# Kernel tuning notes

Measured on AMD Instinct MI355X. Metric: run time of the kernel, lower is better.

Reference implementation:

```python
import jax, jax.numpy as jnp
import numpy as np

D_MODEL = 512
D_K = 64
D_V = 128
H = D_MODEL // D_V  # 4 heads (num_head = d_model // d_v per the source)
B, N = 4, 2048


def setup_inputs() -> dict:
    key = jax.random.key(0)
    k0, k1, k2, k3, k4 = jax.random.split(key, 5)
    s = 0.02
    return {
        "input_x": jax.random.normal(k0, (B, N, D_MODEL), jnp.float32),
        "Wq": jax.random.normal(k1, (D_MODEL, H * D_K), jnp.float32) * s,
        "Wk": jax.random.normal(k2, (D_MODEL, H * D_K), jnp.float32) * s,
        "Wv": jax.random.normal(k3, (D_MODEL, D_MODEL), jnp.float32) * s,
        "Wo": jax.random.normal(k4, (D_MODEL, D_MODEL), jnp.float32) * s,
    }


def reference(input_x, Wq, Wk, Wv, Wo):
    b, n, _ = input_x.shape
    # Contiguous per-head slices in the source == a simple reshape here.
    q = (input_x @ Wq).reshape(b, n, H, D_K)   # [B,N,H,dk]
    k = (input_x @ Wk).reshape(b, n, H, D_K)   # [B,N,H,dk]
    v = (input_x @ Wv).reshape(b, n, H, D_V)   # [B,N,H,dv]
    scale = jnp.sqrt(jnp.float32(D_K))
    scores = jnp.einsum('bqhd,bkhd->bhqk', q, k) / scale  # [B,H,N,N]
    # FAITHFUL quirk: the source uses nn.Softmax() with no dim on a 3D
    # (B,N,N) tensor; PyTorch's legacy dim inference picks dim=0 (batch).
    attn = jax.nn.softmax(scores, axis=0)
    out = jnp.einsum('bhqk,bkhd->bqhd', attn, v).reshape(b, n, H * D_V)
    return out @ Wo
```

## Files before the change

### kernel.cpp

```cpp
#include <hip/hip_runtime.h>
#include <hip/hip_bf16.h>


typedef __attribute__((ext_vector_type(8))) short short8;
typedef __attribute__((ext_vector_type(4))) float floatx4;
typedef unsigned short u16;
typedef unsigned int u32;

#define MFMA16(a, b, c) __builtin_amdgcn_mfma_f32_16x16x32_bf16((a), (b), (c), 0, 0, 0)

__device__ __forceinline__ u16 f2bf(float f) {
    union { float f; unsigned u; } v; v.f = f;
    unsigned r = v.u + 0x7fffu + ((v.u >> 16) & 1u);
    return (u16)(r >> 16);
}

__device__ __forceinline__ float bf2f(u16 b) {
    union { unsigned u; float f; } v; v.u = ((u32)b) << 16;
    return v.f;
}

__device__ __forceinline__ u32 pk2bf(float a, float b) {
#if __has_builtin(__builtin_amdgcn_cvt_pk_bf16_f32)
    typedef __attribute__((ext_vector_type(2))) __bf16 bf16x2;
    union { bf16x2 v; u32 u; } c;
    c.v = __builtin_amdgcn_cvt_pk_bf16_f32(a, b);
    return c.u;
#else
    return (u32)f2bf(a) | ((u32)f2bf(b) << 16);
#endif
}

__device__ __forceinline__ float ex2(float x) {
#if __has_builtin(__builtin_amdgcn_exp2f)
    return __builtin_amdgcn_exp2f(x);
#else
    return exp2f(x);
#endif
}

__device__ __forceinline__ void gload_lds16(const u16* g, u16* l) {
    __builtin_amdgcn_global_load_lds(
        (const __attribute__((address_space(1))) void*)(const void*)g,
        (__attribute__((address_space(3))) void*)(void*)l, 16, 0, 0);
}

__global__ __launch_bounds__(256) void prep_all_kernel(
    const float* __restrict__ x, u16* __restrict__ xb,
    const float* __restrict__ Wq, const float* __restrict__ Wk,
    const float* __restrict__ Wv, const float* __restrict__ Wo,
    u16* __restrict__ WallT, u16* __restrict__ WoT) {
    const int bid = blockIdx.x;
    const int tid = threadIdx.x;
    if (bid < 4096) {
        int i = bid * 256 + tid;
        float4 v = ((const float4*)x)[i];
        ushort4 o;
        o.x = f2bf(v.x); o.y = f2bf(v.y); o.z = f2bf(v.z); o.w = f2bf(v.w);
        ((ushort4*)xb)[i] = o;
        return;
    }
    __shared__ u16 lds[64 * 80];
    const int t = bid - 4096;
    const int k0 = (t & 7) * 64;
    const int n0 = (t >> 3) * 64;
    const float* src; int ld, coff; float scale = 1.0f;
    u16* dst;
    if (n0 < 256)       { src = Wq; ld = 256; coff = n0;        dst = WallT + (size_t)n0 * 512; scale = 0.18033688011f; }
    else if (n0 < 512)  { src = Wk; ld = 256; coff = n0 - 256;  dst = WallT + (size_t)n0 * 512; }
    else if (n0 < 1024) { src = Wv; ld = 512; coff = n0 - 512;  dst = WallT + (size_t)n0 * 512; }
    else                { src = Wo; ld = 512; coff = n0 - 1024; dst = WoT + (size_t)(n0 - 1024) * 512; }
#pragma unroll
    for (int p = 0; p < 4; p++) {
        int r  = (tid >> 4) + p * 16;
        int c4 = (tid & 15) * 4;
        float4 v = *(const float4*)&src[(size_t)(k0 + r) * ld + coff + c4];
        lds[(c4 + 0) * 80 + r] = f2bf(v.x * scale);
        lds[(c4 + 1) * 80 + r] = f2bf(v.y * scale);
        lds[(c4 + 2) * 80 + r] = f2bf(v.z * scale);
        lds[(c4 + 3) * 80 + r] = f2bf(v.w * scale);
    }
    __syncthreads();
#pragma unroll
    for (int p = 0; p < 2; p++) {
        int nn = (tid >> 3) + p * 32;
        int kk = (tid & 7) * 8;
        *(short8*)&dst[(size_t)nn * 512 + k0 + kk] = *(const short8*)&lds[nn * 80 + kk];
    }
}

__global__ __launch_bounds__(512) void gemm_qkv_kernel(
    const u16* __restrict__ A, const u16* __restrict__ BT,
    u16* __restrict__ Qp, u16* __restrict__ Kp, u16* __restrict__ Vp,
    int Kdim) {
    __shared__ u16 sm[16896];
    u16* Asl = sm;
    u16* Bsl = sm + 8192;
    const int tid = threadIdx.x;
    const int bid0 = blockIdx.y * 8 + blockIdx.x;
    const int xcd = bid0 & 7, jj = bid0 >> 3;
    const int mbase = (xcd * 8 + (jj >> 3)) * 128;
    const int nbase = (jj & 7) * 128;
    const int wave = tid >> 6, lane = tid & 63;
    const int wm = wave >> 2, wn = wave & 3;
    const int lq = lane & 15, quad = lane >> 4;

    const int scol = ((lane & 7) ^ (lane >> 3)) * 8;
    const u16* gA = A + (size_t)(mbase + wave * 16 + (lane >> 3)) * Kdim + scol;
    const u16* gB = BT + (size_t)(nbase + wave * 16 + (lane >> 3)) * Kdim + scol;
    u16* lA = &Asl[(wave * 16) * 64];
    u16* lB = &Bsl[(wave * 16) * 64];

    const floatx4 z4 = {0.f, 0.f, 0.f, 0.f};
    floatx4 acc[4][2];
#pragma unroll
    for (int i = 0; i < 4; i++)
#pragma unroll
        for (int j = 0; j < 2; j++) acc[i][j] = z4;

    const int nk = Kdim >> 6;
    for (int kk = 0; kk < nk; kk++) {
        const int kb = kk << 6;
        if (kk) __syncthreads();
#pragma unroll
        for (int i = 0; i < 2; i++) {
            gload_lds16(gA + kb + (size_t)(i * 8) * Kdim, lA + (i * 8) * 64);
            gload_lds16(gB + kb + (size_t)(i * 8) * Kdim, lB + (i * 8) * 64);
        }
        __syncthreads();
#pragma unroll
        for (int ki = 0; ki < 2; ki++) {
            short8 af[4], bf[2];
#pragma unroll
            for (int mi = 0; mi < 4; mi++)
                af[mi] = *(const short8*)&Asl[(wm * 64 + mi * 16 + lq) * 64 +
                                              (((ki * 4 + quad) ^ (lq & 7)) * 8)];
#pragma unroll
            for (int ni = 0; ni < 2; ni++)
                bf[ni] = *(const short8*)&Bsl[(wn * 32 + ni * 16 + lq) * 64 +
                                              (((ki * 4 + quad) ^ (lq & 7)) * 8)];
#pragma unroll
            for (int mi = 0; mi < 4; mi++)
#pragma unroll
                for (int ni = 0; ni < 2; ni++)
                    acc[mi][ni] = MFMA16(af[mi], bf[ni], acc[mi][ni]);
        }
    }
    __syncthreads();
    const bool vtile = (nbase >= 512);
#pragma unroll
    for (int mi = 0; mi < 4; mi++)
#pragma unroll
        for (int ni = 0; ni < 2; ni++) {
            int cl = wn * 32 + ni * 16 + lq;
#pragma unroll
            for (int r = 0; r < 4; r++) {
                int rl = wm * 64 + mi * 16 + quad * 4 + r;
                if (vtile) sm[cl * 132 + rl] = f2bf(acc[mi][ni][r]);
                else       sm[rl * 132 + cl] = f2bf(acc[mi][ni][r]);
            }
        }
    __syncthreads();
    const int b = mbase >> 11;
    const int keyb = mbase & 2047;
    if (nbase < 256) {
        const int hq = nbase >> 6;
        const int qs_base = keyb >> 4;
#pragma unroll
        for (int t = 0; t < 4; t++) {
            int l = wave * 4 + t;
            int qs2 = l >> 2, h2 = (l >> 1) & 1, ki = l & 1;
            int qd = lane >> 4, lqq = lane & 15;
            short8 v = *(const short8*)&sm[(qs2 * 16 + lqq) * 132 + h2 * 64 + ki * 32 + qd * 8];
            int h = hq + h2;
            size_t base = ((size_t)(((b * 4 + h) * 128 + (qs_base + qs2)) * 2 + ki) * 64 + lane) << 3;
            *(short8*)&Qp[base] = v;
        }
    } else if (nbase < 512) {
        const int hb = (nbase - 256) >> 6;
        const int ktb = keyb >> 6;
#pragma unroll
        for (int t = 0; t < 4; t++) {
            int l = wave * 4 + t;
            int kt2 = l >> 4, hf = (l >> 3) & 1, nj = (l >> 2) & 1;
            int h2 = (l >> 1) & 1, ki = l & 1;
            int quadk = lane >> 4, lqk = lane & 15;
            short8 v = *(const short8*)&sm[(kt2 * 64 + hf * 32 + lqk * 2 + nj) * 132 +
                                           h2 * 64 + ki * 32 + quadk * 8];
            int h = hb + h2;
            size_t base = ((size_t)(((((b * 4 + h) * 32 + (ktb + kt2)) * 2 + hf) * 2 + nj)
                                    * 2 + ki) * 64 + lane) << 3;
            *(short8*)&Kp[base] = v;
        }
    } else {
        const int h = (nbase - 512) >> 7;
        const int ktb = keyb >> 6;
#pragma unroll
        for (int t = 0; t < 4; t++) {
            int l = wave * 4 + t;
            int kt2 = l >> 4, hf = (l >> 3) & 1, niv = (l >> 1) & 3, wv = l & 1;
            int quadv = lane >> 4, lqv = lane & 15;
            short8 v = *(const short8*)&sm[(hf * 64 + niv * 16 + lqv) * 132 +
                                           kt2 * 64 + wv * 32 + quadv * 8];
            size_t base = ((size_t)(((((b * 4 + h) * 32 + (ktb + kt2)) * 2 + hf) * 4 + niv)
                                    * 2 + wv) * 64 + lane) << 3;
            *(short8*)&Vp[base] = v;
        }
    }
}

__global__ __launch_bounds__(512) void gemm_out_kernel(
    const u16* __restrict__ A, const u16* __restrict__ BT,
    float* __restrict__ Cf, int Kdim, int ldc) {
    __shared__ u16 Asl[64 * 64];
    __shared__ u16 Bsl[128 * 64];
    const int tid = threadIdx.x;
    const int bid0 = blockIdx.y * 4 + blockIdx.x;
    const int xcd = bid0 & 7, jj = bid0 >> 3;
    const int mbase = (xcd * 16 + (jj >> 2)) * 64;
    const int nbase = (jj & 3) * 128;
    const int wave = tid >> 6, lane = tid & 63;
    const int wm = wave >> 2, wn = wave & 3;
    const int lq = lane & 15, quad = lane >> 4;
    const size_t S = (size_t)8192 * 512;

    const u16* gA = A + (size_t)(mbase + wave * 8 + (lane >> 3)) * Kdim + (lane & 7) * 8;
    const u16* gB = BT + (size_t)(nbase + wave * 16 + (lane >> 3)) * Kdim +
                    (((lane & 7) ^ (lane >> 3)) * 8);
    u16* lAw = &Asl[(wave * 8 + (lane >> 3)) * 64 + (((lane & 7) ^ (lane >> 3)) * 8)];
    u16* lB = &Bsl[(wave * 16) * 64];

    const floatx4 z4 = {0.f, 0.f, 0.f, 0.f};
    floatx4 acc[2][2];
#pragma unroll
    for (int i = 0; i < 2; i++)
#pragma unroll
        for (int j = 0; j < 2; j++) acc[i][j] = z4;

    const int nk = Kdim >> 6;
    for (int kk = 0; kk < nk; kk++) {
        const int kb = kk << 6;
        short8 p0 = *(const short8*)(gA + kb);
        short8 p1 = *(const short8*)(gA + kb + S);
        short8 p2 = *(const short8*)(gA + kb + 2 * S);
        short8 p3 = *(const short8*)(gA + kb + 3 * S);
        if (kk) __syncthreads();
        gload_lds16(gB + kb, lB);
        gload_lds16(gB + kb + (size_t)8 * Kdim, lB + 8 * 64);
        short8 o;
#pragma unroll
        for (int j2 = 0; j2 < 8; j2++) {
            float s = bf2f((u16)p0[j2]) + bf2f((u16)p1[j2]) +
                      bf2f((u16)p2[j2]) + bf2f((u16)p3[j2]);
            o[j2] = (short)f2bf(s);
        }
        *(short8*)lAw = o;
        __syncthreads();
#pragma unroll
        for (int ki = 0; ki < 2; ki++) {
            short8 af[2], bf[2];
#pragma unroll
            for (int mi = 0; mi < 2; mi++)
                af[mi] = *(const short8*)&Asl[(wm * 32 + mi * 16 + lq) * 64 +
                                              (((ki * 4 + quad) ^ (lq & 7)) * 8)];
#pragma unroll
            for (int ni = 0; ni < 2; ni++)
                bf[ni] = *(const short8*)&Bsl[(wn * 32 + ni * 16 + lq) * 64 +
                                              (((ki * 4 + quad) ^ (lq & 7)) * 8)];
#pragma unroll
            for (int mi = 0; mi < 2; mi++)
#pragma unroll
                for (int ni = 0; ni < 2; ni++)
                    acc[mi][ni] = MFMA16(af[mi], bf[ni], acc[mi][ni]);
        }
    }
#pragma unroll
    for (int mi = 0; mi < 2; mi++)
#pragma unroll
        for (int ni = 0; ni < 2; ni++)
#pragma unroll
            for (int r = 0; r < 4; r++)
                Cf[(size_t)(mbase + wm * 32 + mi * 16 + quad * 4 + r) * ldc +
                   (nbase + wn * 32 + ni * 16 + lq)] = acc[mi][ni][r];
}

__global__ __launch_bounds__(512) void attn_kernel(const u16* __restrict__ Qp,
                                                   const u16* __restrict__ Kp,
                                                   const u16* __restrict__ Vp,
                                                   u16* __restrict__ Pp) {
    __shared__ u16 pl[2 * 4 * 4096];
    const int bx = blockIdx.x;
    const int h = bx & 3;
    const int ck = (bx >> 2) & 3;
    const int qt = bx >> 4;
    const int tid = threadIdx.x;
    const int wave = tid >> 6, lane = tid & 63;
    const int mi = wave & 3, half = wave >> 2;
    const int dq = wave;
    const int half_v = dq >> 2, ni_v = dq & 3;
    const int lq = lane & 15, quad = lane >> 4;
    const int qs = qt * 4 + mi;

    short8 aq[4][2];
#pragma unroll
    for (int b = 0; b < 4; b++)
#pragma unroll
        for (int ki = 0; ki < 2; ki++)
            aq[b][ki] = *(const short8*)&Qp[
                ((size_t)((((b * 4 + h) * 128 + qs) * 2 + ki) * 64 + lane) << 3)];

    const floatx4 z4 = {0.f, 0.f, 0.f, 0.f};
    floatx4 oacc[4][4];
#pragma unroll
    for (int b = 0; b < 4; b++)
#pragma unroll
        for (int m2 = 0; m2 < 4; m2++) oacc[b][m2] = z4;

    for (int kt = ck * 8; kt < ck * 8 + 8; kt++) {
        u16* plb = &pl[((kt & 1) * 4 + mi) * 4096];
        u16* plbuf = &pl[(kt & 1) * 4 * 4096];
        floatx4 s[4][2];
#pragma unroll
        for (int b = 0; b < 4; b++) {
            const u16* kb = Kp +
                ((size_t)((((b * 4 + h) * 32 + kt) * 2 + half) * 2) << 10) +
                lane * 8;
#pragma unroll
            for (int nj = 0; nj < 2; nj++) {
                s[b][nj] = z4;
#pragma unroll
                for (int ki = 0; ki < 2; ki++)
                    s[b][nj] = MFMA16(aq[b][ki],
                                      *(const short8*)(kb + (nj * 2 + ki) * 512),
                                      s[b][nj]);
            }
        }
        short8 vf[4][2];
#pragma unroll
        for (int b = 0; b < 4; b++) {
            const u16* vb = Vp +
                ((size_t)(((((b * 4 + h) * 32 + kt) * 2 + half_v) * 4 + ni_v) * 2) << 9) +
                lane * 8;
            vf[b][0] = *(const short8*)vb;
            vf[b][1] = *(const short8*)(vb + 512);
        }
#pragma unroll
        for (int r = 0; r < 4; r++) {
            float e0a = ex2(s[0][0][r]), e0b = ex2(s[0][1][r]);
            float e1a = ex2(s[1][0][r]), e1b = ex2(s[1][1][r]);
            float e2a = ex2(s[2][0][r]), e2b = ex2(s[2][1][r]);
            float e3a = ex2(s[3][0][r]), e3b = ex2(s[3][1][r]);
            float ia = __builtin_amdgcn_rcpf(e0a + e1a + e2a + e3a);
            float ib = __builtin_amdgcn_rcpf(e0b + e1b + e2b + e3b);
            int q = quad * 4 + r;
            int col = (half * 32 + 2 * lq) ^ ((q & 7) * 8);
            *(u32*)&plb[(0 * 16 + q) * 64 + col] = pk2bf(e0a * ia, e0b * ib);
            *(u32*)&plb[(1 * 16 + q) * 64 + col] = pk2bf(e1a * ia, e1b * ib);
            *(u32*)&plb[(2 * 16 + q) * 64 + col] = pk2bf(e2a * ia, e2b * ib);
            *(u32*)&plb[(3 * 16 + q) * 64 + col] = pk2bf(e3a * ia, e3b * ib);
        }
        __syncthreads();
        const int sw = (lq & 7) * 8;
#pragma unroll
        for (int b = 0; b < 4; b++) {
#pragma unroll
            for (int m2 = 0; m2 < 4; m2++) {
                const u16* pm = plbuf + m2 * 4096;
                short8 ap0 = *(const short8*)&pm[(b * 16 + lq) * 64 + ((quad * 8) ^ sw)];
                short8 ap1 = *(const short8*)&pm[(b * 16 + lq) * 64 + ((32 + quad * 8) ^ sw)];
                oacc[b][m2] = MFMA16(ap0, vf[b][0], oacc[b][m2]);
                oacc[b][m2] = MFMA16(ap1, vf[b][1], oacc[b][m2]);
            }
        }
    }
    u16* Pc = Pp + (size_t)ck * (8192 * 512);
#pragma unroll
    for (int b = 0; b < 4; b++)
#pragma unroll
        for (int m2 = 0; m2 < 4; m2++)
#pragma unroll
            for (int r = 0; r < 4; r++)
                Pc[(size_t)(b * 2048 + qt * 64 + m2 * 16 + quad * 4 + r) * 512 +
                   h * 128 + dq * 16 + lq] = f2bf(oacc[b][m2][r]);
}

extern "C" void kernel_launch(void* const* d_in, const int* in_sizes, int n_in,
                              void* d_out, int out_size, void* d_ws, size_t ws_size,
                              hipStream_t stream) {
    const float* x  = (const float*)d_in[0];
    const float* Wq = (const float*)d_in[1];
    const float* Wk = (const float*)d_in[2];
    const float* Wv = (const float*)d_in[3];
    const float* Wo = (const float*)d_in[4];
    float* out = (float*)d_out;

    char* ws = (char*)d_ws;
    u16* Pp    = (u16*)ws;
    u16* Xb    = (u16*)ws;
    u16* WallT = (u16*)(ws + (size_t)8 * 1024 * 1024);
    char* tail = ws + (size_t)32 * 1024 * 1024;
    u16* WoT   = (u16*)tail; tail += (size_t)512 * 512 * 2;
    u16* Qp    = (u16*)tail; tail += (size_t)8192 * 256 * 2;
    u16* Kp    = (u16*)tail; tail += (size_t)8192 * 256 * 2;
    u16* Vp    = (u16*)tail; tail += (size_t)8192 * 512 * 2;

    prep_all_kernel<<<4288, 256, 0, stream>>>(x, Xb, Wq, Wk, Wv, Wo, WallT, WoT);
    gemm_qkv_kernel<<<dim3(8, 64), 512, 0, stream>>>(Xb, WallT, Qp, Kp, Vp, 512);
    attn_kernel<<<512, 512, 0, stream>>>(Qp, Kp, Vp, Pp);
    gemm_out_kernel<<<dim3(4, 128), 512, 0, stream>>>(Pp, WoT, out, 512, 512);
}
```

Baseline: 158.6 us.

## Rebalance attention blocks to 32 query rows with fewer key splits

The attention kernel now gives each block 32 query rows instead of 64 and splits the key range into 2 chunks instead of 4. Within a block, waves cover two key tiles per iteration, each handling a quarter of the 64-key tile per query sub-tile. Each wave now keeps half as many output accumulators and loads V fragments for two key tiles per step. With only two partial results per row, the output projection's A-operand loader sums two partials instead of four, which cuts partial-sum storage and reduction traffic. The cost is more K/V reloads per query, and the launch grid (not shown) must match the new block indexing.

```diff
diff --git a/kernel.cpp b/kernel.cpp
--- a/kernel.cpp
+++ b/kernel.cpp
@@ -242,16 +242,13 @@
         const int kb = kk << 6;
         short8 p0 = *(const short8*)(gA + kb);
         short8 p1 = *(const short8*)(gA + kb + S);
-        short8 p2 = *(const short8*)(gA + kb + 2 * S);
-        short8 p3 = *(const short8*)(gA + kb + 3 * S);
         if (kk) __syncthreads();
         gload_lds16(gB + kb, lB);
         gload_lds16(gB + kb + (size_t)8 * Kdim, lB + 8 * 64);
         short8 o;
 #pragma unroll
         for (int j2 = 0; j2 < 8; j2++) {
-            float s = bf2f((u16)p0[j2]) + bf2f((u16)p1[j2]) +
-                      bf2f((u16)p2[j2]) + bf2f((u16)p3[j2]);
+            float s = bf2f((u16)p0[j2]) + bf2f((u16)p1[j2]);
             o[j2] = (short)f2bf(s);
         }
         *(short8*)lAw = o;
@@ -291,15 +288,17 @@
     __shared__ u16 pl[2 * 4 * 4096];
     const int bx = blockIdx.x;
     const int h = bx & 3;
-    const int ck = (bx >> 2) & 3;
-    const int qt = bx >> 4;
+    const int ck = (bx >> 2) & 1;
+    const int qt = bx >> 3;
     const int tid = threadIdx.x;
     const int wave = tid >> 6, lane = tid & 63;
-    const int mi = wave & 3, half = wave >> 2;
+    const int mi = wave & 1;
+    const int half = (wave >> 1) & 1;
+    const int ktq = wave >> 2;
     const int dq = wave;
     const int half_v = dq >> 2, ni_v = dq & 3;
     const int lq = lane & 15, quad = lane >> 4;
-    const int qs = qt * 4 + mi;
+    const int qs = qt * 2 + mi;
 
     short8 aq[4][2];
 #pragma unroll
@@ -310,15 +309,16 @@
                 ((size_t)((((b * 4 + h) * 128 + qs) * 2 + ki) * 64 + lane) << 3)];
 
     const floatx4 z4 = {0.f, 0.f, 0.f, 0.f};
-    floatx4 oacc[4][4];
+    floatx4 oacc[4][2];
 #pragma unroll
     for (int b = 0; b < 4; b++)
 #pragma unroll
-        for (int m2 = 0; m2 < 4; m2++) oacc[b][m2] = z4;
-
-    for (int kt = ck * 8; kt < ck * 8 + 8; kt++) {
-        u16* plb = &pl[((kt & 1) * 4 + mi) * 4096];
-        u16* plbuf = &pl[(kt & 1) * 4 * 4096];
+        for (int m2 = 0; m2 < 2; m2++) oacc[b][m2] = z4;
+
+    const int ckb = ck * 16;
+    for (int it = 0; it < 8; it++) {
+        const int kt = ckb + it * 2 + ktq;
+        u16* plb = &pl[(((it & 1) * 2 + ktq) * 2 + mi) * 4096];
         floatx4 s[4][2];
 #pragma unroll
         for (int b = 0; b < 4; b++) {
@@ -335,14 +335,18 @@
                                       s[b][nj]);
             }
         }
-        short8 vf[4][2];
-#pragma unroll
-        for (int b = 0; b < 4; b++) {
-            const u16* vb = Vp +
-                ((size_t)(((((b * 4 + h) * 32 + kt) * 2 + half_v) * 4 + ni_v) * 2) << 9) +
-                lane * 8;
-            vf[b][0] = *(const short8*)vb;
-            vf[b][1] = *(const short8*)(vb + 512);
+        short8 vf[2][4][2];
+#pragma unroll
+        for (int kq = 0; kq < 2; kq++) {
+            const int ktv = ckb + it * 2 + kq;
+#pragma unroll
+            for (int b = 0; b < 4; b++) {
+                const u16* vb = Vp +
+                    ((size_t)(((((b * 4 + h) * 32 + ktv) * 2 + half_v) * 4 + ni_v) * 2) << 9) +
+                    lane * 8;
+                vf[kq][b][0] = *(const short8*)vb;
+                vf[kq][b][1] = *(const short8*)(vb + 512);
+            }
         }
 #pragma unroll
         for (int r = 0; r < 4; r++) {
@@ -361,15 +365,19 @@
         }
         __syncthreads();
         const int sw = (lq & 7) * 8;
-#pragma unroll
-        for (int b = 0; b < 4; b++) {
-#pragma unroll
-            for (int m2 = 0; m2 < 4; m2++) {
-                const u16* pm = plbuf + m2 * 4096;
-                short8 ap0 = *(const short8*)&pm[(b * 16 + lq) * 64 + ((quad * 8) ^ sw)];
-                short8 ap1 = *(const short8*)&pm[(b * 16 + lq) * 64 + ((32 + quad * 8) ^ sw)];
-                oacc[b][m2] = MFMA16(ap0, vf[b][0], oacc[b][m2]);
-                oacc[b][m2] = MFMA16(ap1, vf[b][1], oacc[b][m2]);
+        u16* plbase = &pl[(it & 1) * 4 * 4096];
+#pragma unroll
+        for (int kq = 0; kq < 2; kq++) {
+#pragma unroll
+            for (int b = 0; b < 4; b++) {
+#pragma unroll
+                for (int m2 = 0; m2 < 2; m2++) {
+                    const u16* pm = plbase + (kq * 2 + m2) * 4096;
+                    short8 ap0 = *(const short8*)&pm[(b * 16 + lq) * 64 + ((quad * 8) ^ sw)];
+                    short8 ap1 = *(const short8*)&pm[(b * 16 + lq) * 64 + ((32 + quad * 8) ^ sw)];
+                    oacc[b][m2] = MFMA16(ap0, vf[kq][b][0], oacc[b][m2]);
+                    oacc[b][m2] = MFMA16(ap1, vf[kq][b][1], oacc[b][m2]);
+                }
             }
         }
     }
@@ -377,10 +385,10 @@
 #pragma unroll
     for (int b = 0; b < 4; b++)
 #pragma unroll
-        for (int m2 = 0; m2 < 4; m2++)
+        for (int m2 = 0; m2 < 2; m2++)
 #pragma unroll
             for (int r = 0; r < 4; r++)
-                Pc[(size_t)(b * 2048 + qt * 64 + m2 * 16 + quad * 4 + r) * 512 +
+                Pc[(size_t)(b * 2048 + qt * 32 + m2 * 16 + quad * 4 + r) * 512 +
                    h * 128 + dq * 16 + lq] = f2bf(oacc[b][m2][r]);
 }
 
```

Result: no change. 158.6 us (+0.0%).
